# Kernel optimization log

Measured on AMD Instinct MI355X. Metric: run time of the kernel, lower is better.

The kernel has to match this reference:

```python
import jax, jax.numpy as jnp
import numpy as np

N1, N2, P, D = 32, 64, 196, 128


def setup_inputs() -> dict:
    key = jax.random.key(0)
    k1, k2, k3 = jax.random.split(key, 3)
    return {
        "features": jax.random.normal(k1, (N1, P, D), jnp.float32),
        "normal_features": jax.random.normal(k2, (N2, P, D), jnp.float32),
        "background_masks": jax.random.uniform(k3, (N1, P), jnp.float32),
        "PH": 14, "PW": 14, "H": 224, "W": 224,
    }


def _interp1d(x, out_size, axis):
    """1-D bilinear resize along `axis`, matching torch align_corners=False."""
    in_size = x.shape[axis]
    src = jnp.maximum((jnp.arange(out_size) + 0.5) * (in_size / out_size) - 0.5, 0.0)
    i0 = jnp.clip(jnp.floor(src).astype(jnp.int32), 0, in_size - 1)
    i1 = jnp.minimum(i0 + 1, in_size - 1)
    w = (src - i0).astype(x.dtype)
    x0 = jnp.take(x, i0, axis=axis)
    x1 = jnp.take(x, i1, axis=axis)
    shape = [1] * x.ndim
    shape[axis] = out_size
    w = w.reshape(shape)
    return x0 * (1.0 - w) + x1 * w


def reference(features, normal_features, background_masks, PH, PW, H, W):
    # L2-normalize patch features
    f = features / jnp.linalg.norm(features, axis=-1, keepdims=True)      # [N1,P,D]
    nf = normal_features / jnp.linalg.norm(normal_features, axis=-1, keepdims=True)  # [N2,P,D]
    # cdist on unit vectors: ||a-b|| = sqrt(2 - 2 a.b); then /2 as in source
    sim = jnp.einsum('apd,bqd->abpq', f, nf)                              # [N1,N2,P,P]
    dist = jnp.sqrt(jnp.maximum(2.0 - 2.0 * sim, 0.0)) * 0.5
    scores_patch = dist.min(axis=-1)                                      # [N1,N2,P]
    scores_patch = scores_patch * background_masks[:, None, :]
    scores = scores_patch.max(axis=-1)                                    # [N1,N2]
    scores_patch = scores_patch.mean(axis=1)                              # [N1,P]
    n1 = features.shape[0]
    sp = scores_patch.reshape(n1, PH, PW)
    sp = _interp1d(sp, H, axis=1)
    scores_pixel = _interp1d(sp, W, axis=2)                               # [N1,H,W]
    return scores.mean(axis=-1), scores_pixel
```

## Files before the change

kernel.cpp:

```cpp
#include <hip/hip_runtime.h>
#include <hip/hip_fp16.h>

typedef __attribute__((ext_vector_type(8))) short f16x8;
typedef __attribute__((ext_vector_type(8))) _Float16 half8;
typedef __attribute__((ext_vector_type(4))) float f32x4;

__device__ __forceinline__ unsigned short f2h(float x) {
    __half h = __float2half(x);
    unsigned short u;
    __builtin_memcpy(&u, &h, 2);
    return u;
}

__device__ __forceinline__ void gll16(const void* g, void* l) {
    __builtin_amdgcn_global_load_lds(
        (const __attribute__((address_space(1))) unsigned*)g,
        (__attribute__((address_space(3))) unsigned*)l, 16, 0, 0);
}

__global__ __launch_bounds__(256) void norm_kernel(
    const float* __restrict__ feats, const float* __restrict__ nfeats,
    unsigned short* __restrict__ fH, unsigned short* __restrict__ nfH)
{
    int row  = blockIdx.x * 4 + (threadIdx.x >> 6);
    int lane = threadIdx.x & 63;
    const float* src;
    unsigned short* dst;
    if (row < 6272) { src = feats  + (size_t)row * 128; dst = fH  + (size_t)row * 128; }
    else { int r2 = row - 6272; src = nfeats + (size_t)r2 * 128; dst = nfH + (size_t)r2 * 128; }

    float2 v = *(const float2*)(src + lane * 2);
    float ss = v.x * v.x + v.y * v.y;
    #pragma unroll
    for (int m = 1; m < 64; m <<= 1) ss += __shfl_xor(ss, m, 64);
    float rn = rsqrtf(ss);
    ushort2 o; o.x = f2h(v.x * rn); o.y = f2h(v.y * rn);
    *(ushort2*)(dst + lane * 2) = o;
}

__device__ __forceinline__ void stage196(const f16x8* __restrict__ g, f16x8* l,
                                         int tid, int wave) {
    #pragma unroll
    for (int i = 0; i < 6; ++i) {
        int slot = i * 512 + tid;
        int row = slot >> 4, cc = slot & 15;
        gll16(g + row * 16 + (cc ^ (row & 7)), l + i * 512 + wave * 64);
    }
    if (tid < 64) {
        int slot = 3072 + tid;
        int row = slot >> 4, cc = slot & 15;
        gll16(g + row * 16 + (cc ^ (row & 7)), l + 3072);
    }
}

__global__ __launch_bounds__(512, 4) void simmax_kernel(
    const unsigned short* __restrict__ fH, const unsigned short* __restrict__ nfH,
    const float* __restrict__ mask, float* __restrict__ sp, float* __restrict__ scores)
{
    __shared__ f16x8 Bl[3136];
    __shared__ unsigned smaxL[4 * 208];
    __shared__ unsigned scoresL[4];

    int blk = blockIdx.x;
    int a = blk >> 4, bq = blk & 15;
    int b0 = bq * 4;
    int tid = threadIdx.x, wave = tid >> 6, lane = tid & 63;
    int l15 = lane & 15, lg = lane >> 4;
    int pg = wave & 3, qh = wave >> 2;
    const int p0tab[4] = {0, 64, 128, 132};
    int p0 = p0tab[pg];
    int qi0 = qh ? 7 : 0, qi1 = qh ? 13 : 7;

    for (int i = tid; i < 4 * 208; i += 512) smaxL[i] = 0u;
    if (tid < 4) scoresL[tid] = 0u;

    const unsigned short* fb = fH + (size_t)a * 196 * 128 + l15 * 128 + lg * 8;
    half8 pb[4][4];
    #pragma unroll
    for (int pt = 0; pt < 4; ++pt) {
        #pragma unroll
        for (int ks = 0; ks < 4; ++ks) {
            const unsigned short* ad = fb + (p0 + pt * 16) * 128 + ks * 32;
            asm volatile("global_load_dwordx4 %0, %1, off" : "=&v"(pb[pt][ks]) : "v"(ad));
        }
    }
    asm volatile("s_waitcnt vmcnt(0)"
        : "+v"(pb[0][0]), "+v"(pb[0][1]), "+v"(pb[0][2]), "+v"(pb[0][3]),
          "+v"(pb[1][0]), "+v"(pb[1][1]), "+v"(pb[1][2]), "+v"(pb[1][3]),
          "+v"(pb[2][0]), "+v"(pb[2][1]), "+v"(pb[2][2]), "+v"(pb[2][3]),
          "+v"(pb[3][0]), "+v"(pb[3][1]), "+v"(pb[3][2]), "+v"(pb[3][3]));
    __builtin_amdgcn_sched_barrier(0);

    for (int bi = 0; bi < 4; ++bi) {
        if (bi > 0) __syncthreads();
        stage196((const f16x8*)(nfH + (size_t)(b0 + bi) * 196 * 128), Bl, tid, wave);
        __syncthreads();

        float rmax[4];
        #pragma unroll
        for (int pt = 0; pt < 4; ++pt) rmax[pt] = -3.0f;

        for (int qi = qi0; qi < qi1; ++qi) {
            int qbase = (qi < 12) ? qi * 16 : 180;
            f32x4 acc[4];
            #pragma unroll
            for (int pt = 0; pt < 4; ++pt) acc[pt] = (f32x4){0.f, 0.f, 0.f, 0.f};
            #pragma unroll
            for (int ks = 0; ks < 4; ++ks) {
                int row = qbase + l15;
                half8 qa = *(const half8*)(Bl + ((row << 4) | ((ks * 4 + lg) ^ (row & 7))));
                #pragma unroll
                for (int pt = 0; pt < 4; ++pt)
                    acc[pt] = __builtin_amdgcn_mfma_f32_16x16x32_f16(qa, pb[pt][ks], acc[pt], 0, 0, 0);
            }
            #pragma unroll
            for (int pt = 0; pt < 4; ++pt)
                rmax[pt] = fmaxf(rmax[pt],
                           fmaxf(fmaxf(acc[pt][0], acc[pt][1]),
                                 fmaxf(acc[pt][2], acc[pt][3])));
        }
        #pragma unroll
        for (int pt = 0; pt < 4; ++pt) {
            float v = rmax[pt];
            v = fmaxf(v, __shfl_xor(v, 16, 64));
            v = fmaxf(v, __shfl_xor(v, 32, 64));
            if (lg == 0)
                atomicMax(&smaxL[bi * 208 + p0 + pt * 16 + l15],
                          __float_as_uint(v + 3.0f));
        }
    }
    __syncthreads();

    if (tid < 256) {
        int p = tid;
        float mk = (p < 196) ? mask[a * 196 + p] : 0.0f;
        float d4[4];
        #pragma unroll
        for (int bi = 0; bi < 4; ++bi) {
            float d = 0.0f;
            if (p < 196) {
                float sim = __uint_as_float(smaxL[bi * 208 + p]) - 3.0f;
                d = 0.5f * sqrtf(fmaxf(2.0f - 2.0f * sim, 0.0f)) * mk;
            }
            d4[bi] = d;
            float m = d;
            #pragma unroll
            for (int s = 1; s < 64; s <<= 1) m = fmaxf(m, __shfl_xor(m, s, 64));
            if (lane == 0) atomicMax(&scoresL[bi], __float_as_uint(m));
        }
        if (p < 196)
            *(f32x4*)(sp + ((size_t)a * 196 + p) * 64 + b0) = (f32x4){d4[0], d4[1], d4[2], d4[3]};
    }
    __syncthreads();
    if (tid < 4)
        scores[a * 64 + b0 + tid] = __uint_as_float(scoresL[tid]);
}

__global__ __launch_bounds__(256) void patchmean_kernel(
    const float* __restrict__ sp, const float* __restrict__ scores,
    float* __restrict__ patch, float* __restrict__ out)
{
    int a = blockIdx.x, tid = threadIdx.x;
    if (tid < 196) {
        const f32x4* v = (const f32x4*)(sp + ((size_t)a * 196 + tid) * 64);
        float s = 0.0f;
        #pragma unroll
        for (int j = 0; j < 16; ++j) { f32x4 x = v[j]; s += x[0] + x[1] + x[2] + x[3]; }
        patch[a * 196 + tid] = s * (1.0f / 64.0f);
    }
    if (tid >= 192 && tid < 256) {
        int l = tid - 192;
        float s = scores[a * 64 + l];
        #pragma unroll
        for (int m = 1; m < 64; m <<= 1) s += __shfl_xor(s, m, 64);
        if (l == 0) out[a] = s * (1.0f / 64.0f);
    }
}

__global__ __launch_bounds__(256) void upsample_kernel(
    const float* __restrict__ patch, float* __restrict__ out)
{
    int bid = blockIdx.x;
    int a = bid / 28, band = bid % 28;
    __shared__ float pt[196];
    if (threadIdx.x < 196) pt[threadIdx.x] = patch[a * 196 + threadIdx.x];
    __syncthreads();

    float* op = out + 32 + (size_t)a * 50176 + band * 8 * 224;
    for (int t = threadIdx.x; t < 8 * 224; t += 256) {
        int h = band * 8 + (t / 224), w = t % 224;
        float sh = fmaxf((h + 0.5f) * 0.0625f - 0.5f, 0.0f);
        float sw = fmaxf((w + 0.5f) * 0.0625f - 0.5f, 0.0f);
        int h0 = (int)sh, w0 = (int)sw;
        int h1 = min(h0 + 1, 13), w1 = min(w0 + 1, 13);
        float fh = sh - (float)h0, fw = sw - (float)w0;
        float v00 = pt[h0 * 14 + w0], v01 = pt[h0 * 14 + w1];
        float v10 = pt[h1 * 14 + w0], v11 = pt[h1 * 14 + w1];
        op[t] = (1.0f - fh) * ((1.0f - fw) * v00 + fw * v01)
              +         fh  * ((1.0f - fw) * v10 + fw * v11);
    }
}

extern "C" void kernel_launch(void* const* d_in, const int* in_sizes, int n_in,
                              void* d_out, int out_size, void* d_ws, size_t ws_size,
                              hipStream_t stream) {
    const float* feats  = (const float*)d_in[0];
    const float* nfeats = (const float*)d_in[1];
    const float* mask   = (const float*)d_in[2];
    float* out = (float*)d_out;

    char* w = (char*)d_ws;
    unsigned short* fH  = (unsigned short*)(w);
    unsigned short* nfH = (unsigned short*)(w + 1605632);
    float* sp     = (float*)(w + 4816896);
    float* scores = (float*)(w + 6422528);
    float* patch  = (float*)(w + 6430720);

    norm_kernel<<<4704, 256, 0, stream>>>(feats, nfeats, fH, nfH);
    simmax_kernel<<<512, 512, 0, stream>>>(fH, nfH, mask, sp, scores);
    patchmean_kernel<<<32, 256, 0, stream>>>(sp, scores, patch, out);
    upsample_kernel<<<896, 256, 0, stream>>>(patch, out);
}
```

Measured before the change: 52.16 us.

## Double-buffer normal-feature staging with 1024-thread blocks covering 8 normals

```diff
diff --git a/kernel.cpp b/kernel.cpp
--- a/kernel.cpp
+++ b/kernel.cpp
@@ -38,13 +38,13 @@
     *(ushort2*)(dst + lane * 2) = o;
 }
 
-__device__ __forceinline__ void stage196(const f16x8* __restrict__ g, f16x8* l,
-                                         int tid, int wave) {
+__device__ __forceinline__ void stage1024(const f16x8* __restrict__ g, f16x8* l,
+                                          int tid, int wave) {
     #pragma unroll
-    for (int i = 0; i < 6; ++i) {
-        int slot = i * 512 + tid;
+    for (int i = 0; i < 3; ++i) {
+        int slot = i * 1024 + tid;
         int row = slot >> 4, cc = slot & 15;
-        gll16(g + row * 16 + (cc ^ (row & 7)), l + i * 512 + wave * 64);
+        gll16(g + row * 16 + (cc ^ (row & 7)), l + i * 1024 + wave * 64);
     }
     if (tid < 64) {
         int slot = 3072 + tid;
@@ -53,26 +53,26 @@
     }
 }
 
-__global__ __launch_bounds__(512, 4) void simmax_kernel(
+__global__ __launch_bounds__(1024, 4) void simmax_kernel(
     const unsigned short* __restrict__ fH, const unsigned short* __restrict__ nfH,
     const float* __restrict__ mask, float* __restrict__ sp, float* __restrict__ scores)
 {
-    __shared__ f16x8 Bl[3136];
-    __shared__ unsigned smaxL[4 * 208];
-    __shared__ unsigned scoresL[4];
-
-    int blk = blockIdx.x;
-    int a = blk >> 4, bq = blk & 15;
-    int b0 = bq * 4;
+    __shared__ f16x8 Bbuf[2][3136];
+    __shared__ unsigned smaxL[8 * 208];
+    __shared__ unsigned scoresL[8];
+
+    int a = blockIdx.x & 31, bg = blockIdx.x >> 5;
+    int b0 = bg * 8;
     int tid = threadIdx.x, wave = tid >> 6, lane = tid & 63;
     int l15 = lane & 15, lg = lane >> 4;
-    int pg = wave & 3, qh = wave >> 2;
+    int pg = wave & 3, qs = wave >> 2;
     const int p0tab[4] = {0, 64, 128, 132};
     int p0 = p0tab[pg];
-    int qi0 = qh ? 7 : 0, qi1 = qh ? 13 : 7;
-
-    for (int i = tid; i < 4 * 208; i += 512) smaxL[i] = 0u;
-    if (tid < 4) scoresL[tid] = 0u;
+    const int qstart[4] = {0, 4, 7, 10};
+    const int qend[4]   = {4, 7, 10, 13};
+
+    for (int i = tid; i < 8 * 208; i += 1024) smaxL[i] = 0u;
+    if (tid < 8) scoresL[tid] = 0u;
 
     const unsigned short* fb = fH + (size_t)a * 196 * 128 + l15 * 128 + lg * 8;
     half8 pb[4][4];
@@ -91,16 +91,20 @@
           "+v"(pb[3][0]), "+v"(pb[3][1]), "+v"(pb[3][2]), "+v"(pb[3][3]));
     __builtin_amdgcn_sched_barrier(0);
 
-    for (int bi = 0; bi < 4; ++bi) {
-        if (bi > 0) __syncthreads();
-        stage196((const f16x8*)(nfH + (size_t)(b0 + bi) * 196 * 128), Bl, tid, wave);
-        __syncthreads();
+    stage1024((const f16x8*)(nfH + (size_t)b0 * 196 * 128), Bbuf[0], tid, wave);
+    __syncthreads();
+
+    for (int bi = 0; bi < 8; ++bi) {
+        f16x8* Bcur = Bbuf[bi & 1];
+        f16x8* Bnxt = Bbuf[(bi & 1) ^ 1];
+        if (bi < 7)
+            stage1024((const f16x8*)(nfH + (size_t)(b0 + bi + 1) * 196 * 128), Bnxt, tid, wave);
 
         float rmax[4];
         #pragma unroll
         for (int pt = 0; pt < 4; ++pt) rmax[pt] = -3.0f;
 
-        for (int qi = qi0; qi < qi1; ++qi) {
+        for (int qi = qstart[qs]; qi < qend[qs]; ++qi) {
             int qbase = (qi < 12) ? qi * 16 : 180;
             f32x4 acc[4];
             #pragma unroll
@@ -108,7 +112,7 @@
             #pragma unroll
             for (int ks = 0; ks < 4; ++ks) {
                 int row = qbase + l15;
-                half8 qa = *(const half8*)(Bl + ((row << 4) | ((ks * 4 + lg) ^ (row & 7))));
+                half8 qa = *(const half8*)(Bcur + ((row << 4) | ((ks * 4 + lg) ^ (row & 7))));
                 #pragma unroll
                 for (int pt = 0; pt < 4; ++pt)
                     acc[pt] = __builtin_amdgcn_mfma_f32_16x16x32_f16(qa, pb[pt][ks], acc[pt], 0, 0, 0);
@@ -128,31 +132,34 @@
                 atomicMax(&smaxL[bi * 208 + p0 + pt * 16 + l15],
                           __float_as_uint(v + 3.0f));
         }
-    }
-    __syncthreads();
+        __syncthreads();
+    }
 
     if (tid < 256) {
         int p = tid;
         float mk = (p < 196) ? mask[a * 196 + p] : 0.0f;
-        float d4[4];
-        #pragma unroll
-        for (int bi = 0; bi < 4; ++bi) {
+        float d8[8];
+        #pragma unroll
+        for (int bi = 0; bi < 8; ++bi) {
             float d = 0.0f;
             if (p < 196) {
                 float sim = __uint_as_float(smaxL[bi * 208 + p]) - 3.0f;
                 d = 0.5f * sqrtf(fmaxf(2.0f - 2.0f * sim, 0.0f)) * mk;
             }
-            d4[bi] = d;
+            d8[bi] = d;
             float m = d;
             #pragma unroll
             for (int s = 1; s < 64; s <<= 1) m = fmaxf(m, __shfl_xor(m, s, 64));
             if (lane == 0) atomicMax(&scoresL[bi], __float_as_uint(m));
         }
-        if (p < 196)
-            *(f32x4*)(sp + ((size_t)a * 196 + p) * 64 + b0) = (f32x4){d4[0], d4[1], d4[2], d4[3]};
+        if (p < 196) {
+            float* dst = sp + ((size_t)a * 196 + p) * 64 + b0;
+            *(f32x4*)(dst)     = (f32x4){d8[0], d8[1], d8[2], d8[3]};
+            *(f32x4*)(dst + 4) = (f32x4){d8[4], d8[5], d8[6], d8[7]};
+        }
     }
     __syncthreads();
-    if (tid < 4)
+    if (tid < 8)
         scores[a * 64 + b0 + tid] = __uint_as_float(scoresL[tid]);
 }
 
@@ -217,7 +224,7 @@
     float* patch  = (float*)(w + 6430720);
 
     norm_kernel<<<4704, 256, 0, stream>>>(feats, nfeats, fH, nfH);
-    simmax_kernel<<<512, 512, 0, stream>>>(fH, nfH, mask, sp, scores);
+    simmax_kernel<<<256, 1024, 0, stream>>>(fH, nfH, mask, sp, scores);
     patchmean_kernel<<<32, 256, 0, stream>>>(sp, scores, patch, out);
     upsample_kernel<<<896, 256, 0, stream>>>(patch, out);
 }
```

After: 56.46 us. 8.2% more time.
